# Kernel tuning notes

Hardware: AMD Instinct MI355X
Metric: run time of the kernel (lower is better)

## Reference

```python
import jax, jax.numpy as jnp
import numpy as np

H, DK, DV = 8, 64, 64
BETA = 0.5
EPS = 1e-5


def _pe(length, d):
    # standard sinusoidal positional encoding, (length, d)
    pos = np.arange(length, dtype=np.float32)[:, None]
    i = np.arange(0, d, 2, dtype=np.float32)
    ang = pos / np.power(10000.0, i / d)
    pe = np.zeros((length, d), dtype=np.float32)
    pe[:, 0::2] = np.sin(ang)
    pe[:, 1::2] = np.cos(ang)
    return jnp.asarray(pe)


def _ln(x, g, b):
    m = x.mean(-1, keepdims=True)
    v = ((x - m) ** 2).mean(-1, keepdims=True)
    return (x - m) / jnp.sqrt(v + EPS) * g + b


def _mha(q_in, k_in, v_in, wq, bq, wk, bk, wv, bv, wo, bo):
    # meshed-memory style MHA; attention_mask is all-ones in this module -> no-op
    B, Sq, _ = q_in.shape
    Sk = k_in.shape[1]
    q = (q_in @ wq + bq).reshape(B, Sq, H, DK).transpose(0, 2, 1, 3)
    k = (k_in @ wk + bk).reshape(B, Sk, H, DK).transpose(0, 2, 1, 3)
    v = (v_in @ wv + bv).reshape(B, Sk, H, DV).transpose(0, 2, 1, 3)
    att = jax.nn.softmax(jnp.einsum('bhqd,bhkd->bhqk', q, k) / np.float32(np.sqrt(DK)), axis=-1)
    out = jnp.einsum('bhqk,bhkd->bhqd', att, v).transpose(0, 2, 1, 3).reshape(B, Sq, H * DV)
    return out @ wo + bo, att


def setup_inputs() -> dict:
    key = jax.random.key(0)
    ks = jax.random.split(key, 24)
    d, n_e = 512, 64
    B, S_enc, T = 16, 1024, 2048
    s = 0.02
    inp = {
        'x_enc': jax.random.normal(ks[0], (B, S_enc, d), jnp.float32),
        'z': jax.random.normal(ks[1], (B, T, d), jnp.float32),
        'emb_table': jax.random.normal(ks[2], (n_e, d), jnp.float32),
    }
    names = ['sha_wq', 'sha_wk', 'sha_wv', 'sha_wo', 'esha_wq', 'esha_wk', 'esha_wv', 'esha_wo']
    for i, n in enumerate(names):
        inp[n] = jax.random.normal(ks[3 + i], (d, d), jnp.float32) * s
        inp[n.replace('w', 'b')] = jnp.zeros((d,), jnp.float32)
    inp['esha_ln_g'] = jnp.ones((d,), jnp.float32)
    inp['esha_ln_b'] = jnp.zeros((d,), jnp.float32)
    inp['norm_g'] = jnp.ones((d,), jnp.float32)
    inp['norm_b'] = jnp.zeros((d,), jnp.float32)
    return inp


def reference(x_enc, z, emb_table, sha_wq, sha_bq, sha_wk, sha_bk, sha_wv, sha_bv, sha_wo, sha_bo,
              esha_wq, esha_bq, esha_wk, esha_bk, esha_wv, esha_bv, esha_wo, esha_bo,
              esha_ln_g, esha_ln_b, norm_g, norm_b):
    B = x_enc.shape[0]
    n_e, d = emb_table.shape
    # --- create_conditioned_embedding ---
    emb = jnp.broadcast_to(emb_table[None], (B, n_e, d)) + _pe(n_e, d)[None]
    y, _ = _mha(emb, x_enc, x_enc, sha_wq, sha_bq, sha_wk, sha_bk, sha_wv, sha_bv, sha_wo, sha_bo)
    emb = _ln(emb + y, norm_g, norm_b)
    y2, _ = _mha(emb, emb, emb, esha_wq, esha_bq, esha_wk, esha_bk, esha_wv, esha_bv, esha_wo, esha_bo)
    emb = _ln(emb + y2, esha_ln_g, esha_ln_b)  # proj = Identity (d_proj == d_model)
    # --- vqvae_min_encodings: squared distances (B, T, n_e) ---
    d2 = ((z * z).sum(-1)[:, :, None] + (emb * emb).sum(-1)[:, None, :]
          - 2.0 * jnp.einsum('btd,bkd->btk', z, emb))
    idx = jnp.argmin(d2, axis=-1)                      # (B, T)
    enc = jax.nn.one_hot(idx, n_e, dtype=z.dtype)      # (B, T, n_e)
    # --- extract_zq: one-hot gather via matmul ---
    z_q = jnp.einsum('btk,bkd->btd', enc, emb)
    sg = jax.lax.stop_gradient
    loss = (BETA * jnp.mean((sg(z_q) - z) ** 2) + jnp.mean((z_q - sg(z)) ** 2)).reshape(1)
    z_q = z + sg(z_q - z)  # straight-through
    e_mean = enc.reshape(-1, n_e).mean(0)
    perplexity = jnp.exp(-jnp.sum(e_mean * jnp.log(e_mean + 1e-10)))
    return z_q, loss, perplexity, enc.reshape(-1, n_e), idx, emb
```

## Files before the change

### kernel.cpp

```cpp
#include <hip/hip_runtime.h>
#include <math.h>

#define DD     512
#define NBATCH 16
#define SENC   1024
#define TTOK   2048
#define NHEAD  8
#define HDIM   64
#define NE     64

#define WS_K1    0
#define WS_V1    (WS_K1 + NBATCH*SENC*DD)
#define WS_EMB0  (WS_V1 + NBATCH*SENC*DD)
#define WS_Q1    (WS_EMB0 + NE*DD)
#define WS_ATT1  (WS_Q1 + NE*DD)
#define WS_EMB1  (WS_ATT1 + NBATCH*NE*DD)
#define WS_Q2    (WS_EMB1 + NBATCH*NE*DD)
#define WS_K2    (WS_Q2 + NBATCH*NE*DD)
#define WS_V2    (WS_K2 + NBATCH*NE*DD)
#define WS_ATT2  (WS_V2 + NBATCH*NE*DD)
#define WS_YBUF  (WS_ATT2 + NBATCH*NE*DD)
#define WS_EMBF  (WS_YBUF + NBATCH*NE*DD)
#define WS_E2    (WS_EMBF + NBATCH*NE*DD)
#define WS_LOSSP (WS_E2 + 2*NBATCH*NE)
#define WS_CNT   (WS_LOSSP + 2*512)

#define OUT_ZQ   0
#define OUT_LOSS (NBATCH*TTOK*DD)
#define OUT_PERP (OUT_LOSS + 1)
#define OUT_ENC  (OUT_PERP + 1)
#define OUT_IDX  (OUT_ENC + NBATCH*TTOK*NE)
#define OUT_EMB  (OUT_IDX + NBATCH*TTOK)

__global__ __launch_bounds__(256) void pe_emb0_k(const float* __restrict__ tab,
                                                 float* __restrict__ emb0)
{
    int p = blockIdx.x;
    for (int c = threadIdx.x; c < DD; c += 256) {
        int ie = c & ~1;
        float denom = (float)pow(10000.0, (double)ie / 512.0);
        float ang = (float)p / denom;
        double v = (c & 1) ? cos((double)ang) : sin((double)ang);
        emb0[p * DD + c] = tab[p * DD + c] + (float)v;
    }
}

template <int NOUT>
__global__ __launch_bounds__(256) void gemm_bias_k(
    const float* __restrict__ A,
    const float* __restrict__ W0, const float* __restrict__ B0, float* __restrict__ C0,
    const float* __restrict__ W1, const float* __restrict__ B1, float* __restrict__ C1,
    const float* __restrict__ W2, const float* __restrict__ B2, float* __restrict__ C2)
{
    __shared__ float As[32][64];
    __shared__ float Ws[NOUT][32][64];
    const int m0 = blockIdx.x * 64;
    const int n0 = blockIdx.y * 64;
    const int tid = threadIdx.x;
    const int tx = tid & 15, ty = tid >> 4;

    float acc[NOUT][4][4];
#pragma unroll
    for (int o = 0; o < NOUT; ++o)
#pragma unroll
        for (int i = 0; i < 4; ++i)
#pragma unroll
            for (int j = 0; j < 4; ++j) acc[o][i][j] = 0.f;

    const float* Wp[3] = {W0, W1, W2};

    for (int kk = 0; kk < DD; kk += 32) {
        __syncthreads();
#pragma unroll
        for (int l = 0; l < 2; ++l) {
            int fid = l * 256 + tid;
            int row = fid >> 3, c4 = fid & 7;
            float4 v = *reinterpret_cast<const float4*>(&A[(size_t)(m0 + row) * DD + kk + c4 * 4]);
            As[c4 * 4 + 0][row] = v.x;
            As[c4 * 4 + 1][row] = v.y;
            As[c4 * 4 + 2][row] = v.z;
            As[c4 * 4 + 3][row] = v.w;
        }
#pragma unroll
        for (int o = 0; o < NOUT; ++o) {
#pragma unroll
            for (int l = 0; l < 2; ++l) {
                int fid = l * 256 + tid;
                int kr = fid >> 4, c4 = fid & 15;
                *reinterpret_cast<float4*>(&Ws[o][kr][c4 * 4]) =
                    *reinterpret_cast<const float4*>(&Wp[o][(size_t)(kk + kr) * DD + n0 + c4 * 4]);
            }
        }
        __syncthreads();
#pragma unroll
        for (int k = 0; k < 32; ++k) {
            float4 av = *reinterpret_cast<const float4*>(&As[k][ty * 4]);
            float a[4] = {av.x, av.y, av.z, av.w};
#pragma unroll
            for (int o = 0; o < NOUT; ++o) {
                float4 wv = *reinterpret_cast<const float4*>(&Ws[o][k][tx * 4]);
#pragma unroll
                for (int i = 0; i < 4; ++i) {
                    acc[o][i][0] = fmaf(a[i], wv.x, acc[o][i][0]);
                    acc[o][i][1] = fmaf(a[i], wv.y, acc[o][i][1]);
                    acc[o][i][2] = fmaf(a[i], wv.z, acc[o][i][2]);
                    acc[o][i][3] = fmaf(a[i], wv.w, acc[o][i][3]);
                }
            }
        }
    }
    float* Cp[3] = {C0, C1, C2};
    const float* Bp[3] = {B0, B1, B2};
#pragma unroll
    for (int o = 0; o < NOUT; ++o) {
#pragma unroll
        for (int i = 0; i < 4; ++i) {
            int row = m0 + ty * 4 + i;
#pragma unroll
            for (int j = 0; j < 4; ++j) {
                int col = n0 + tx * 4 + j;
                Cp[o][(size_t)row * DD + col] = acc[o][i][j] + Bp[o][col];
            }
        }
    }
}

__global__ __launch_bounds__(256) void attn_k(
    const float* __restrict__ q, int q_shared,
    const float* __restrict__ kmat, const float* __restrict__ vmat,
    float* __restrict__ outp, int slen)
{
    __shared__ float qs[64][68];
    __shared__ float kst[64][68];
    __shared__ float vs[64][68];
    int b = blockIdx.x >> 3, h = blockIdx.x & 7;
    int tid = threadIdx.x;
    const float* qb = q + (q_shared ? (size_t)0 : (size_t)b * 64 * DD);
    const float* kb = kmat + (size_t)b * slen * DD;
    const float* vb = vmat + (size_t)b * slen * DD;

#pragma unroll
    for (int l = 0; l < 4; ++l) {
        int fid = l * 256 + tid;
        int r = fid >> 4, c4 = fid & 15;
        *reinterpret_cast<float4*>(&qs[r][c4 * 4]) =
            *reinterpret_cast<const float4*>(&qb[(size_t)r * DD + h * HDIM + c4 * 4]);
    }
    const int row = tid >> 2, c4 = tid & 3;
    float acc[16];
#pragma unroll
    for (int i = 0; i < 16; ++i) acc[i] = 0.f;
    float m_run = -INFINITY, l_run = 0.f;

    for (int s0 = 0; s0 < slen; s0 += 64) {
        __syncthreads();
#pragma unroll
        for (int l = 0; l < 4; ++l) {
            int fid = l * 256 + tid;
            int r = fid >> 4, cc = fid & 15;
            float4 t4 = *reinterpret_cast<const float4*>(&kb[(size_t)(s0 + r) * DD + h * HDIM + cc * 4]);
            kst[cc * 4 + 0][r] = t4.x;
            kst[cc * 4 + 1][r] = t4.y;
            kst[cc * 4 + 2][r] = t4.z;
            kst[cc * 4 + 3][r] = t4.w;
            *reinterpret_cast<float4*>(&vs[r][cc * 4]) =
                *reinterpret_cast<const float4*>(&vb[(size_t)(s0 + r) * DD + h * HDIM + cc * 4]);
        }
        __syncthreads();

        float p[16];
#pragma unroll
        for (int i = 0; i < 16; ++i) p[i] = 0.f;
#pragma unroll 4
        for (int e = 0; e < 64; ++e) {
            float qv = qs[row][e];
#pragma unroll
            for (int j4 = 0; j4 < 4; ++j4) {
                float4 k4 = *reinterpret_cast<const float4*>(&kst[e][c4 * 16 + j4 * 4]);
                p[j4 * 4 + 0] = fmaf(qv, k4.x, p[j4 * 4 + 0]);
                p[j4 * 4 + 1] = fmaf(qv, k4.y, p[j4 * 4 + 1]);
                p[j4 * 4 + 2] = fmaf(qv, k4.z, p[j4 * 4 + 2]);
                p[j4 * 4 + 3] = fmaf(qv, k4.w, p[j4 * 4 + 3]);
            }
        }
#pragma unroll
        for (int i = 0; i < 16; ++i) p[i] *= 0.125f;
        float mx = p[0];
#pragma unroll
        for (int i = 1; i < 16; ++i) mx = fmaxf(mx, p[i]);
        mx = fmaxf(mx, __shfl_xor(mx, 1));
        mx = fmaxf(mx, __shfl_xor(mx, 2));
        float m_new = fmaxf(m_run, mx);
        float scale = expf(m_run - m_new);
        float lsum = 0.f;
#pragma unroll
        for (int i = 0; i < 16; ++i) { p[i] = expf(p[i] - m_new); lsum += p[i]; }
        lsum += __shfl_xor(lsum, 1);
        lsum += __shfl_xor(lsum, 2);
        l_run = l_run * scale + lsum;
        m_run = m_new;
#pragma unroll
        for (int i = 0; i < 16; ++i) acc[i] *= scale;

#pragma unroll 16
        for (int j = 0; j < 64; ++j) {
            float pv = __shfl(p[j & 15], j >> 4, 4);
#pragma unroll
            for (int u = 0; u < 4; ++u) {
                float4 v4 = *reinterpret_cast<const float4*>(&vs[j][c4 * 16 + u * 4]);
                acc[u * 4 + 0] = fmaf(pv, v4.x, acc[u * 4 + 0]);
                acc[u * 4 + 1] = fmaf(pv, v4.y, acc[u * 4 + 1]);
                acc[u * 4 + 2] = fmaf(pv, v4.z, acc[u * 4 + 2]);
                acc[u * 4 + 3] = fmaf(pv, v4.w, acc[u * 4 + 3]);
            }
        }
    }
#pragma unroll
    for (int i = 0; i < 16; ++i) acc[i] /= l_run;
#pragma unroll
    for (int u = 0; u < 4; ++u) {
        float4 o4 = {acc[u * 4 + 0], acc[u * 4 + 1], acc[u * 4 + 2], acc[u * 4 + 3]};
        *reinterpret_cast<float4*>(&outp[((size_t)b * 64 + row) * DD + h * HDIM + c4 * 16 + u * 4]) = o4;
    }
}

__device__ __forceinline__ float block_sum256(float v, float* sb)
{
#pragma unroll
    for (int off = 32; off; off >>= 1) v += __shfl_down(v, off);
    __syncthreads();
    if ((threadIdx.x & 63) == 0) sb[threadIdx.x >> 6] = v;
    __syncthreads();
    return (sb[0] + sb[1]) + (sb[2] + sb[3]);
}

__global__ __launch_bounds__(256) void ln_k(
    const float* __restrict__ res, int res_shared, const float* __restrict__ y,
    const float* __restrict__ g, const float* __restrict__ bb,
    float* __restrict__ out, float* __restrict__ out2, double* __restrict__ e2)
{
    __shared__ float sbuf[4];
    __shared__ double dbuf[4];
    int row = blockIdx.x;
    int t = threadIdx.x;
    const float* rp = res + (size_t)(res_shared ? (row & 63) : row) * DD;
    const float* yp = y + (size_t)row * DD;
    float x0 = rp[t] + yp[t];
    float x1 = rp[t + 256] + yp[t + 256];
    float m = block_sum256(x0 + x1, sbuf) / 512.0f;
    float d0 = x0 - m, d1 = x1 - m;
    float v = block_sum256(d0 * d0 + d1 * d1, sbuf) / 512.0f;
    float s = sqrtf(v + 1e-5f);
    float o0 = d0 / s * g[t] + bb[t];
    float o1 = d1 / s * g[t + 256] + bb[t + 256];
    out[(size_t)row * DD + t] = o0;
    out[(size_t)row * DD + t + 256] = o1;
    if (out2) {
        out2[(size_t)row * DD + t] = o0;
        out2[(size_t)row * DD + t + 256] = o1;
    }
    if (e2) {
        double sd = (double)o0 * o0 + (double)o1 * o1;
#pragma unroll
        for (int off = 32; off; off >>= 1) sd += __shfl_down(sd, off);
        if ((t & 63) == 0) dbuf[t >> 6] = sd;
        __syncthreads();
        if (t == 0) e2[row] = (dbuf[0] + dbuf[1]) + (dbuf[2] + dbuf[3]);
    }
}

__global__ __launch_bounds__(512) void vq_k(
    const float* __restrict__ z, const float* __restrict__ emb,
    const double* __restrict__ e2,
    float* __restrict__ zq, float* __restrict__ enc, float* __restrict__ idxo,
    double* __restrict__ lossp, int* __restrict__ counts)
{
    __shared__ float zs[32][68];
    __shared__ float es[32][68];
    __shared__ int   kms[64];
    __shared__ double dred[8];
    __shared__ int   cnt_s[64];

    const int bid = blockIdx.x;
    const int b   = bid >> 5;
    const int m0  = (bid & 31) * 64;
    const int tid = threadIdx.x;
    const int tx  = tid & 15, ty = tid >> 4;

    const float* zb = z   + ((size_t)b * TTOK + m0) * DD;
    const float* eb = emb + (size_t)b * NE * DD;

    double acc[2][4];
#pragma unroll
    for (int r = 0; r < 2; ++r)
#pragma unroll
        for (int j = 0; j < 4; ++j) acc[r][j] = 0.0;

    const int lrow = tid >> 3, lc4 = tid & 7;

    for (int kk = 0; kk < DD; kk += 32) {
        __syncthreads();
        {
            float4 t4 = *reinterpret_cast<const float4*>(&zb[(size_t)lrow * DD + kk + lc4 * 4]);
            zs[lc4 * 4 + 0][lrow] = t4.x;
            zs[lc4 * 4 + 1][lrow] = t4.y;
            zs[lc4 * 4 + 2][lrow] = t4.z;
            zs[lc4 * 4 + 3][lrow] = t4.w;
            float4 e4 = *reinterpret_cast<const float4*>(&eb[(size_t)lrow * DD + kk + lc4 * 4]);
            es[lc4 * 4 + 0][lrow] = e4.x;
            es[lc4 * 4 + 1][lrow] = e4.y;
            es[lc4 * 4 + 2][lrow] = e4.z;
            es[lc4 * 4 + 3][lrow] = e4.w;
        }
        __syncthreads();
#pragma unroll
        for (int k = 0; k < 32; ++k) {
            float2 zv = *reinterpret_cast<const float2*>(&zs[k][ty * 2]);
            float4 ev = *reinterpret_cast<const float4*>(&es[k][tx * 4]);
            double z0 = (double)zv.x, z1 = (double)zv.y;
            double e0 = (double)ev.x, e1 = (double)ev.y;
            double e2d = (double)ev.z, e3 = (double)ev.w;
            acc[0][0] = fma(z0, e0, acc[0][0]);
            acc[0][1] = fma(z0, e1, acc[0][1]);
            acc[0][2] = fma(z0, e2d, acc[0][2]);
            acc[0][3] = fma(z0, e3, acc[0][3]);
            acc[1][0] = fma(z1, e0, acc[1][0]);
            acc[1][1] = fma(z1, e1, acc[1][1]);
            acc[1][2] = fma(z1, e2d, acc[1][2]);
            acc[1][3] = fma(z1, e3, acc[1][3]);
        }
    }

    double e2v[4];
#pragma unroll
    for (int j = 0; j < 4; ++j) e2v[j] = e2[b * NE + tx * 4 + j];

    double vmin[2]; int imin[2];
#pragma unroll
    for (int r = 0; r < 2; ++r) {
        vmin[r] = e2v[0] - 2.0 * acc[r][0];
        imin[r] = tx * 4;
#pragma unroll
        for (int j = 1; j < 4; ++j) {
            double s = e2v[j] - 2.0 * acc[r][j];
            if (s < vmin[r]) { vmin[r] = s; imin[r] = tx * 4 + j; }
        }
    }
#pragma unroll
    for (int off = 1; off < 16; off <<= 1) {
#pragma unroll
        for (int r = 0; r < 2; ++r) {
            double ov = __shfl_xor(vmin[r], off);
            int    oi = __shfl_xor(imin[r], off);
            if (ov < vmin[r] || (ov == vmin[r] && oi < imin[r])) { vmin[r] = ov; imin[r] = oi; }
        }
    }
    if (tid < 64) cnt_s[tid] = 0;
    if (tx == 0) { kms[ty * 2] = imin[0]; kms[ty * 2 + 1] = imin[1]; }
    __syncthreads();
    if (tid < 64) atomicAdd(&cnt_s[kms[tid]], 1);

    const int row = tid >> 3, p = tid & 7;
    const int km  = kms[row];
    const float* zr = &zb[(size_t)row * DD];
    const float* er = &eb[(size_t)km * DD];
    const size_t grow = (size_t)b * TTOK + m0 + row;
    float* zqr = zq + grow * DD;
    double lsum = 0.0;
#pragma unroll 4
    for (int i = 0; i < 16; ++i) {
        int col = (i * 8 + p) * 4;
        float4 zv = *reinterpret_cast<const float4*>(&zr[col]);
        float4 ev = *reinterpret_cast<const float4*>(&er[col]);
        float d0 = ev.x - zv.x, d1 = ev.y - zv.y, d2 = ev.z - zv.z, d3 = ev.w - zv.w;
        lsum += (double)d0 * d0 + (double)d1 * d1 + (double)d2 * d2 + (double)d3 * d3;
        float4 o4 = {zv.x + d0, zv.y + d1, zv.z + d2, zv.w + d3};
        *reinterpret_cast<float4*>(&zqr[col]) = o4;
    }
    {
        float* ep = enc + grow * NE + p * 8;
        float4 o0, o1;
        o0.x = (p * 8 + 0 == km) ? 1.f : 0.f;
        o0.y = (p * 8 + 1 == km) ? 1.f : 0.f;
        o0.z = (p * 8 + 2 == km) ? 1.f : 0.f;
        o0.w = (p * 8 + 3 == km) ? 1.f : 0.f;
        o1.x = (p * 8 + 4 == km) ? 1.f : 0.f;
        o1.y = (p * 8 + 5 == km) ? 1.f : 0.f;
        o1.z = (p * 8 + 6 == km) ? 1.f : 0.f;
        o1.w = (p * 8 + 7 == km) ? 1.f : 0.f;
        *reinterpret_cast<float4*>(ep)     = o0;
        *reinterpret_cast<float4*>(ep + 4) = o1;
    }
    if (tid < 64) idxo[(size_t)b * TTOK + m0 + tid] = (float)kms[tid];

#pragma unroll
    for (int off = 32; off; off >>= 1) lsum += __shfl_down(lsum, off);
    if ((tid & 63) == 0) dred[tid >> 6] = lsum;
    __syncthreads();
    if (tid == 0) {
        double t = 0.0;
#pragma unroll
        for (int w = 0; w < 8; ++w) t += dred[w];
        lossp[bid] = t;
    }
    if (tid < 64 && cnt_s[tid]) atomicAdd(&counts[tid], cnt_s[tid]);
}

__global__ void fin_k(const double* __restrict__ lossp, const int* __restrict__ counts,
                      float* __restrict__ loss_out, float* __restrict__ perp_out)
{
    int tid = threadIdx.x;
    if (tid == 0) {
        double tot = 0.0;
        for (int i = 0; i < 512; ++i) tot += lossp[i];
        loss_out[0] = (float)(1.5 * tot / 16777216.0);
    }
    float e = counts[tid] / 32768.0f;
    float term = e * logf(e + 1e-10f);
#pragma unroll
    for (int off = 32; off; off >>= 1) term += __shfl_down(term, off);
    if (tid == 0) perp_out[0] = expf(-term);
}

extern "C" void kernel_launch(void* const* d_in, const int* in_sizes, int n_in,
                              void* d_out, int out_size, void* d_ws, size_t ws_size,
                              hipStream_t stream)
{
    (void)in_sizes; (void)n_in; (void)out_size; (void)ws_size;
    const float* x_enc = (const float*)d_in[0];
    const float* z     = (const float*)d_in[1];
    const float* tab   = (const float*)d_in[2];
    const float* wq1 = (const float*)d_in[3];  const float* bq1 = (const float*)d_in[4];
    const float* wk1 = (const float*)d_in[5];  const float* bk1 = (const float*)d_in[6];
    const float* wv1 = (const float*)d_in[7];  const float* bv1 = (const float*)d_in[8];
    const float* wo1 = (const float*)d_in[9];  const float* bo1 = (const float*)d_in[10];
    const float* wq2 = (const float*)d_in[11]; const float* bq2 = (const float*)d_in[12];
    const float* wk2 = (const float*)d_in[13]; const float* bk2 = (const float*)d_in[14];
    const float* wv2 = (const float*)d_in[15]; const float* bv2 = (const float*)d_in[16];
    const float* wo2 = (const float*)d_in[17]; const float* bo2 = (const float*)d_in[18];
    const float* ln2g = (const float*)d_in[19]; const float* ln2b = (const float*)d_in[20];
    const float* ln1g = (const float*)d_in[21]; const float* ln1b = (const float*)d_in[22];

    float* ws  = (float*)d_ws;
    float* out = (float*)d_out;

    float* k1   = ws + WS_K1;
    float* v1   = ws + WS_V1;
    float* emb0 = ws + WS_EMB0;
    float* q1   = ws + WS_Q1;
    float* att1 = ws + WS_ATT1;
    float* emb1 = ws + WS_EMB1;
    float* q2   = ws + WS_Q2;
    float* k2   = ws + WS_K2;
    float* v2   = ws + WS_V2;
    float* att2 = ws + WS_ATT2;
    float* ybuf = ws + WS_YBUF;
    float* embf = ws + WS_EMBF;
    double* e2    = (double*)(ws + WS_E2);
    double* lossp = (double*)(ws + WS_LOSSP);
    int*    cnts  = (int*)(ws + WS_CNT);

    hipMemsetAsync(cnts, 0, NE * sizeof(int), stream);

    pe_emb0_k<<<64, 256, 0, stream>>>(tab, emb0);

    gemm_bias_k<1><<<dim3(1, 8), 256, 0, stream>>>(emb0, wq1, bq1, q1,
                                                   nullptr, nullptr, nullptr,
                                                   nullptr, nullptr, nullptr);
    gemm_bias_k<2><<<dim3(256, 8), 256, 0, stream>>>(x_enc, wk1, bk1, k1,
                                                     wv1, bv1, v1,
                                                     nullptr, nullptr, nullptr);
    attn_k<<<128, 256, 0, stream>>>(q1, 1, k1, v1, att1, SENC);

    gemm_bias_k<1><<<dim3(16, 8), 256, 0, stream>>>(att1, wo1, bo1, ybuf,
                                                    nullptr, nullptr, nullptr,
                                                    nullptr, nullptr, nullptr);
    ln_k<<<1024, 256, 0, stream>>>(emb0, 1, ybuf, ln1g, ln1b, emb1, nullptr, nullptr);

    gemm_bias_k<3><<<dim3(16, 8), 256, 0, stream>>>(emb1, wq2, bq2, q2,
                                                    wk2, bk2, k2,
                                                    wv2, bv2, v2);
    attn_k<<<128, 256, 0, stream>>>(q2, 0, k2, v2, att2, 64);

    gemm_bias_k<1><<<dim3(16, 8), 256, 0, stream>>>(att2, wo2, bo2, ybuf,
                                                    nullptr, nullptr, nullptr,
                                                    nullptr, nullptr, nullptr);
    ln_k<<<1024, 256, 0, stream>>>(emb1, 0, ybuf, ln2g, ln2b, embf, out + OUT_EMB, e2);

    vq_k<<<512, 512, 0, stream>>>(z, embf, e2,
                                  out + OUT_ZQ, out + OUT_ENC, out + OUT_IDX,
                                  lossp, cnts);
    fin_k<<<1, 64, 0, stream>>>(lossp, cnts, out + OUT_LOSS, out + OUT_PERP);
}
```

Before: 610.1 us.

## Replace K/V projection GEMM with wave-per-tile kernel and split attention query rows

```diff
diff --git a/kernel.cpp b/kernel.cpp
--- a/kernel.cpp
+++ b/kernel.cpp
@@ -45,6 +45,52 @@
     }
 }
 
+__global__ __launch_bounds__(256) void gemm_kv_k(
+    const float* __restrict__ A,
+    const float* __restrict__ W0, const float* __restrict__ B0, float* __restrict__ C0,
+    const float* __restrict__ W1, const float* __restrict__ B1, float* __restrict__ C1)
+{
+    const int lane  = threadIdx.x & 63;
+    const int wslot = __builtin_amdgcn_readfirstlane(threadIdx.x >> 6);
+    const int wid   = blockIdx.x * 4 + wslot;
+    const int nt     = wid >> 10;
+    const int mchunk = wid & 1023;
+    const int n0 = nt * 64;
+    const int m0 = mchunk * 16;
+
+    const float* Ab = A + (size_t)m0 * DD;
+
+    float acc0[16], acc1[16];
+#pragma unroll
+    for (int r = 0; r < 16; ++r) { acc0[r] = 0.f; acc1[r] = 0.f; }
+
+    for (int kk = 0; kk < DD; kk += 32) {
+        float w0[32], w1[32];
+#pragma unroll
+        for (int j = 0; j < 32; ++j) {
+            w0[j] = W0[(size_t)(kk + j) * DD + n0 + lane];
+            w1[j] = W1[(size_t)(kk + j) * DD + n0 + lane];
+        }
+#pragma unroll
+        for (int r = 0; r < 16; ++r) {
+            float a[32];
+#pragma unroll
+            for (int j = 0; j < 32; ++j) a[j] = Ab[(size_t)r * DD + kk + j];
+#pragma unroll
+            for (int j = 0; j < 32; ++j) {
+                acc0[r] = fmaf(a[j], w0[j], acc0[r]);
+                acc1[r] = fmaf(a[j], w1[j], acc1[r]);
+            }
+        }
+    }
+    float b0 = B0[n0 + lane], b1 = B1[n0 + lane];
+#pragma unroll
+    for (int r = 0; r < 16; ++r) {
+        C0[(size_t)(m0 + r) * DD + n0 + lane] = acc0[r] + b0;
+        C1[(size_t)(m0 + r) * DD + n0 + lane] = acc1[r] + b1;
+    }
+}
+
 template <int NOUT>
 __global__ __launch_bounds__(256) void gemm_bias_k(
     const float* __restrict__ A,
@@ -125,15 +171,16 @@
     }
 }
 
-__global__ __launch_bounds__(256) void attn_k(
+__global__ __launch_bounds__(128) void attn_k(
     const float* __restrict__ q, int q_shared,
     const float* __restrict__ kmat, const float* __restrict__ vmat,
     float* __restrict__ outp, int slen)
 {
-    __shared__ float qs[64][68];
+    __shared__ float qs[32][68];
     __shared__ float kst[64][68];
     __shared__ float vs[64][68];
-    int b = blockIdx.x >> 3, h = blockIdx.x & 7;
+    int bid = blockIdx.x;
+    int b = bid >> 4, h = (bid >> 1) & 7, half = bid & 1;
     int tid = threadIdx.x;
     const float* qb = q + (q_shared ? (size_t)0 : (size_t)b * 64 * DD);
     const float* kb = kmat + (size_t)b * slen * DD;
@@ -141,10 +188,10 @@
 
 #pragma unroll
     for (int l = 0; l < 4; ++l) {
-        int fid = l * 256 + tid;
+        int fid = l * 128 + tid;
         int r = fid >> 4, c4 = fid & 15;
         *reinterpret_cast<float4*>(&qs[r][c4 * 4]) =
-            *reinterpret_cast<const float4*>(&qb[(size_t)r * DD + h * HDIM + c4 * 4]);
+            *reinterpret_cast<const float4*>(&qb[(size_t)(half * 32 + r) * DD + h * HDIM + c4 * 4]);
     }
     const int row = tid >> 2, c4 = tid & 3;
     float acc[16];
@@ -155,8 +202,8 @@
     for (int s0 = 0; s0 < slen; s0 += 64) {
         __syncthreads();
 #pragma unroll
-        for (int l = 0; l < 4; ++l) {
-            int fid = l * 256 + tid;
+        for (int l = 0; l < 8; ++l) {
+            int fid = l * 128 + tid;
             int r = fid >> 4, cc = fid & 15;
             float4 t4 = *reinterpret_cast<const float4*>(&kb[(size_t)(s0 + r) * DD + h * HDIM + cc * 4]);
             kst[cc * 4 + 0][r] = t4.x;
@@ -220,7 +267,7 @@
 #pragma unroll
     for (int u = 0; u < 4; ++u) {
         float4 o4 = {acc[u * 4 + 0], acc[u * 4 + 1], acc[u * 4 + 2], acc[u * 4 + 3]};
-        *reinterpret_cast<float4*>(&outp[((size_t)b * 64 + row) * DD + h * HDIM + c4 * 16 + u * 4]) = o4;
+        *reinterpret_cast<float4*>(&outp[((size_t)b * 64 + half * 32 + row) * DD + h * HDIM + c4 * 16 + u * 4]) = o4;
     }
 }
 
@@ -467,10 +514,9 @@
     gemm_bias_k<1><<<dim3(1, 8), 256, 0, stream>>>(emb0, wq1, bq1, q1,
                                                    nullptr, nullptr, nullptr,
                                                    nullptr, nullptr, nullptr);
-    gemm_bias_k<2><<<dim3(256, 8), 256, 0, stream>>>(x_enc, wk1, bk1, k1,
-                                                     wv1, bv1, v1,
-                                                     nullptr, nullptr, nullptr);
-    attn_k<<<128, 256, 0, stream>>>(q1, 1, k1, v1, att1, SENC);
+    gemm_kv_k<<<2048, 256, 0, stream>>>(x_enc, wk1, bk1, k1,
+                                        wv1, bv1, v1);
+    attn_k<<<256, 128, 0, stream>>>(q1, 1, k1, v1, att1, SENC);
 
     gemm_bias_k<1><<<dim3(16, 8), 256, 0, stream>>>(att1, wo1, bo1, ybuf,
                                                     nullptr, nullptr, nullptr,
@@ -480,7 +526,7 @@
     gemm_bias_k<3><<<dim3(16, 8), 256, 0, stream>>>(emb1, wq2, bq2, q2,
                                                     wk2, bk2, k2,
                                                     wv2, bv2, v2);
-    attn_k<<<128, 256, 0, stream>>>(q2, 0, k2, v2, att2, 64);
+    attn_k<<<256, 128, 0, stream>>>(q2, 0, k2, v2, att2, 64);
 
     gemm_bias_k<1><<<dim3(16, 8), 256, 0, stream>>>(att2, wo2, bo2, ybuf,
                                                     nullptr, nullptr, nullptr,
```

After: 921.1 us. 51.0% more time.
